# Optimization experiments

Hardware: AMD Instinct MI355X
Metric: run time of the kernel (lower is better)

Reference implementation:

```python
import jax, jax.numpy as jnp
import numpy as np

EPS_MAG = 1e-6    # magnitude threshold for valid trajectory
EPS_WSUM = 1e-8   # clamp on combined weight sum


def setup_inputs() -> dict:
    key = jax.random.key(0)
    embeddings = jax.random.normal(key, (4, 4096, 1024), dtype=jnp.float32)
    return {"embeddings": embeddings, "max_trajectory_distance": 8}


def reference(embeddings, max_trajectory_distance):
    # Vectorized form of compute_sparse_trajectories:
    # for each pos p >= 1, window of diffs d[start..p-1], start = max(0, p - max_dist),
    # normalized diffs weighted by linspace(0.1, 1.0, window) * tanh(2*|d|),
    # output[p] = weighted sum / clamp(weight sum, 1e-8); output[0] = 0.
    B, S, D = embeddings.shape
    maxd = min(int(max_trajectory_distance), S - 1)

    d = embeddings[:, 1:, :] - embeddings[:, :-1, :]            # [B, S-1, D]
    mag = jnp.linalg.norm(d, axis=-1)                           # [B, S-1]
    normed = jnp.where((mag > EPS_MAG)[..., None],
                       d / jnp.maximum(mag, EPS_MAG)[..., None],
                       0.0)                                     # [B, S-1, D]
    magw = jnp.tanh(mag * 2.0)                                  # [B, S-1]

    p = jnp.arange(S)                                           # positions
    wsize = jnp.minimum(maxd, p)                                # window size per pos
    j = jnp.arange(maxd)
    idx = p[:, None] - maxd + j[None, :]                        # [S, maxd] diff indices (end-aligned)
    valid = idx >= 0                                            # [S, maxd]
    # k = rank within window (0..wsize-1): weights linspace(0.1, 1.0, wsize)
    k = (j[None, :] - (maxd - wsize)[:, None]).astype(jnp.float32)
    denom = jnp.maximum(wsize - 1, 1).astype(jnp.float32)[:, None]
    lin = jnp.where(wsize[:, None] > 1, 0.1 + 0.9 * k / denom, 0.1)
    lin = jnp.where(valid, lin, 0.0)                            # [S, maxd]

    ci = jnp.clip(idx, 0, S - 2)                                # safe gather indices
    n_g = normed[:, ci, :]                                      # [B, S, maxd, D]
    m_g = magw[:, ci]                                           # [B, S, maxd]
    comb = lin[None, :, :] * m_g * valid[None, :, :]            # combined weights

    wsum = jnp.maximum(comb.sum(axis=-1), EPS_WSUM)             # [B, S]
    traj = jnp.einsum('bsjd,bsj->bsd', n_g, comb) / wsum[..., None]
    return traj
```

## Files before the change

### kernel.cpp

```cpp
#include <hip/hip_runtime.h>
#include <hip/hip_bf16.h>


constexpr int B_ = 4;
constexpr int S_ = 4096;
constexpr int D_ = 1024;
constexpr int MAXD  = 8;
constexpr int CHUNK = 32;
constexpr int ROWS  = CHUNK + MAXD;
constexpr int NDIFF = ROWS - 1;
constexpr int NCHUNK = S_ / CHUNK;
constexpr int NWG    = NCHUNK * B_;
constexpr int NXCD   = 8;

__global__ __launch_bounds__(256, 2)
void traj_splat_kernel(const float* __restrict__ emb, float* __restrict__ out) {
    const int bid = blockIdx.x;
    const int lin = (bid % NXCD) * (NWG / NXCD) + bid / NXCD;
    const int schunk = lin & (NCHUNK - 1);
    const int b      = lin >> 7;

    const int s0   = schunk * CHUNK;
    const int lane = threadIdx.x & 63;
    const int wave = threadIdx.x >> 6;
    const int d0   = threadIdx.x * 4;

    const float* __restrict__ embB = emb + (size_t)b * S_ * D_;

    __shared__ float part[NDIFF][4][4];
    __shared__ float smagw[NDIFF];
    __shared__ float sq[NDIFF];
    __shared__ float gco[CHUNK][12];

    float4 win[ROWS];
    #pragma unroll
    for (int r = 0; r < ROWS; ++r) {
        const int row = s0 - MAXD + r;
        if (row >= 0)
            win[r] = *(const float4*)(embB + (size_t)row * D_ + d0);
        else
            win[r] = make_float4(0.f, 0.f, 0.f, 0.f);
    }

    #pragma unroll
    for (int li = 0; li < NDIFF; ++li) {
        const float4 a = win[li], c = win[li + 1];
        const float dx = c.x - a.x, dy = c.y - a.y;
        const float dz = c.z - a.z, dw = c.w - a.w;
        float sum = dx * dx + dy * dy + dz * dz + dw * dw;
        sum += __shfl_xor(sum, 32, 64);
        sum += __shfl_xor(sum, 16, 64);
        sum += __shfl_xor(sum,  8, 64);
        sum += __shfl_xor(sum,  4, 64);
        if (lane < 4) part[li][wave][lane] = sum;
    }
    __syncthreads();

    if (threadIdx.x < NDIFF) {
        const int li = threadIdx.x;
        float s2 = 0.f;
        #pragma unroll
        for (int w = 0; w < 4; ++w)
            #pragma unroll
            for (int k = 0; k < 4; ++k)
                s2 += part[li][w][k];
        const float mag = sqrtf(s2);
        const float mw  = tanhf(2.f * mag);
        smagw[li] = mw;
        sq[li]    = (mag > 1e-6f) ? (mw / mag) : 0.f;
    }
    __syncthreads();

    if (threadIdx.x < CHUNK) {
        const int sl = threadIdx.x;
        const int s  = s0 + sl;
        const int ws = min(MAXD, s);
        const int lo = MAXD - ws;
        const float rden = 0.9f / (float)max(ws - 1, 1);

        float cpad[MAXD + 2];
        #pragma unroll
        for (int t = 0; t < MAXD + 2; ++t) cpad[t] = 0.f;

        float wsum = 0.f;
        #pragma unroll
        for (int j = 0; j < MAXD; ++j) {
            if (j >= lo) {
                const int li = sl + j;
                const float lin2 = (ws > 1) ? (0.1f + rden * (float)(j - lo)) : 0.1f;
                wsum += lin2 * smagw[li];
                cpad[j + 1] = lin2 * sq[li];
            }
        }
        const float inv = 1.f / fmaxf(wsum, 1e-8f);
        #pragma unroll
        for (int jr = 0; jr <= MAXD; ++jr)
            gco[sl][jr] = (cpad[jr] - cpad[jr + 1]) * inv;
    }
    __syncthreads();

    float* outB = out + ((size_t)b * S_ + s0) * D_ + d0;
    #pragma unroll
    for (int sl = 0; sl < CHUNK; ++sl) {
        const float4 g0 = *(const float4*)&gco[sl][0];
        const float4 g1 = *(const float4*)&gco[sl][4];
        const float  g8 = gco[sl][8];

        float4 acc;
        acc.x = g0.x * win[sl].x; acc.y = g0.x * win[sl].y;
        acc.z = g0.x * win[sl].z; acc.w = g0.x * win[sl].w;
        const float gs[8] = {g0.y, g0.z, g0.w, g1.x, g1.y, g1.z, g1.w, g8};
        #pragma unroll
        for (int jr = 1; jr <= MAXD; ++jr) {
            const float g = gs[jr - 1];
            acc.x += g * win[sl + jr].x;
            acc.y += g * win[sl + jr].y;
            acc.z += g * win[sl + jr].z;
            acc.w += g * win[sl + jr].w;
        }
        *(float4*)(outB + (size_t)sl * D_) = acc;
    }
}

extern "C" void kernel_launch(void* const* d_in, const int* in_sizes, int n_in,
                              void* d_out, int out_size, void* d_ws, size_t ws_size,
                              hipStream_t stream) {
    const float* emb = (const float*)d_in[0];
    float* out = (float*)d_out;

    dim3 grid(NWG);
    dim3 block(256);
    traj_splat_kernel<<<grid, block, 0, stream>>>(emb, out);
}
```

Before: 29.71 us.

## Split into magnitude pre-pass and splat kernel to drop halo recompute

Splits the fused kernel in two. A first pass computes each diff's magnitude weight and scale once and writes them to the workspace. A second kernel uses smaller 16-row chunks, reads those per-diff scalars from global memory, and does the weighted splat. This removes the redundant norm reductions over halo rows and allows higher occupancy, at the cost of an extra launch, a second full read of the embeddings, and a dependency on workspace size, with a fallback to the old fused kernel when the workspace is too small.

```diff
diff --git a/kernel.cpp b/kernel.cpp
--- a/kernel.cpp
+++ b/kernel.cpp
@@ -5,45 +5,36 @@
 constexpr int B_ = 4;
 constexpr int S_ = 4096;
 constexpr int D_ = 1024;
-constexpr int MAXD  = 8;
-constexpr int CHUNK = 32;
-constexpr int ROWS  = CHUNK + MAXD;
-constexpr int NDIFF = ROWS - 1;
-constexpr int NCHUNK = S_ / CHUNK;
-constexpr int NWG    = NCHUNK * B_;
-constexpr int NXCD   = 8;
+constexpr int MAXD = 8;
+constexpr int NDIFF_TOT = S_ - 1;
+
+constexpr int K1_CHUNK = 32;
 
 __global__ __launch_bounds__(256, 2)
-void traj_splat_kernel(const float* __restrict__ emb, float* __restrict__ out) {
-    const int bid = blockIdx.x;
-    const int lin = (bid % NXCD) * (NWG / NXCD) + bid / NXCD;
-    const int schunk = lin & (NCHUNK - 1);
-    const int b      = lin >> 7;
-
-    const int s0   = schunk * CHUNK;
+void mag_kernel(const float* __restrict__ emb,
+                float* __restrict__ magw_g, float* __restrict__ q_g) {
+    const int r0 = blockIdx.x * K1_CHUNK;
+    const int b  = blockIdx.y;
     const int lane = threadIdx.x & 63;
     const int wave = threadIdx.x >> 6;
     const int d0   = threadIdx.x * 4;
 
     const float* __restrict__ embB = emb + (size_t)b * S_ * D_;
 
-    __shared__ float part[NDIFF][4][4];
-    __shared__ float smagw[NDIFF];
-    __shared__ float sq[NDIFF];
-    __shared__ float gco[CHUNK][12];
-
-    float4 win[ROWS];
-    #pragma unroll
-    for (int r = 0; r < ROWS; ++r) {
-        const int row = s0 - MAXD + r;
-        if (row >= 0)
+    __shared__ float part[K1_CHUNK][4][4];
+
+    float4 win[K1_CHUNK + 1];
+    #pragma unroll
+    for (int r = 0; r <= K1_CHUNK; ++r) {
+        const int row = r0 + r;
+        if (row < S_)
             win[r] = *(const float4*)(embB + (size_t)row * D_ + d0);
         else
             win[r] = make_float4(0.f, 0.f, 0.f, 0.f);
     }
 
     #pragma unroll
-    for (int li = 0; li < NDIFF; ++li) {
+    for (int li = 0; li < K1_CHUNK; ++li) {
         const float4 a = win[li], c = win[li + 1];
         const float dx = c.x - a.x, dy = c.y - a.y;
         const float dz = c.z - a.z, dw = c.w - a.w;
@@ -56,7 +47,159 @@
     }
     __syncthreads();
 
-    if (threadIdx.x < NDIFF) {
+    if (threadIdx.x < K1_CHUNK) {
+        const int li = threadIdx.x;
+        const int d  = r0 + li;
+        if (d < NDIFF_TOT) {
+            float s2 = 0.f;
+            #pragma unroll
+            for (int w = 0; w < 4; ++w)
+                #pragma unroll
+                for (int k = 0; k < 4; ++k)
+                    s2 += part[li][w][k];
+            const float mag = sqrtf(s2);
+            const float mw  = tanhf(2.f * mag);
+            const size_t o  = (size_t)b * NDIFF_TOT + d;
+            magw_g[o] = mw;
+            q_g[o]    = (mag > 1e-6f) ? (mw / mag) : 0.f;
+        }
+    }
+}
+
+constexpr int CHUNK2  = 16;
+constexpr int ROWS2   = CHUNK2 + MAXD;
+constexpr int NCHUNK2 = S_ / CHUNK2;
+constexpr int NWG2    = NCHUNK2 * B_;
+constexpr int NXCD    = 8;
+
+__global__ __launch_bounds__(256, 3)
+void splat_kernel(const float* __restrict__ emb,
+                  const float* __restrict__ magw_g, const float* __restrict__ q_g,
+                  float* __restrict__ out) {
+    const int bid = blockIdx.x;
+    const int lin = (bid % NXCD) * (NWG2 / NXCD) + bid / NXCD;
+    const int schunk = lin & (NCHUNK2 - 1);
+    const int b      = lin >> 8;
+
+    const int s0 = schunk * CHUNK2;
+    const int d0 = threadIdx.x * 4;
+
+    const float* __restrict__ embB = emb + (size_t)b * S_ * D_;
+
+    __shared__ float gco[CHUNK2][12];
+
+    float4 win[ROWS2];
+    #pragma unroll
+    for (int r = 0; r < ROWS2; ++r) {
+        const int row = s0 - MAXD + r;
+        if (row >= 0)
+            win[r] = *(const float4*)(embB + (size_t)row * D_ + d0);
+        else
+            win[r] = make_float4(0.f, 0.f, 0.f, 0.f);
+    }
+
+    if (threadIdx.x < CHUNK2) {
+        const int sl = threadIdx.x;
+        const int s  = s0 + sl;
+        const int ws = min(MAXD, s);
+        const int lo = MAXD - ws;
+        const float rden = 0.9f / (float)max(ws - 1, 1);
+        const size_t bD  = (size_t)b * NDIFF_TOT;
+
+        float cpad[MAXD + 2];
+        #pragma unroll
+        for (int t = 0; t < MAXD + 2; ++t) cpad[t] = 0.f;
+
+        float wsum = 0.f;
+        #pragma unroll
+        for (int j = 0; j < MAXD; ++j) {
+            if (j >= lo) {
+                const int d = s - MAXD + j;
+                const float lin2 = (ws > 1) ? (0.1f + rden * (float)(j - lo)) : 0.1f;
+                wsum += lin2 * magw_g[bD + d];
+                cpad[j + 1] = lin2 * q_g[bD + d];
+            }
+        }
+        const float inv = 1.f / fmaxf(wsum, 1e-8f);
+        #pragma unroll
+        for (int jr = 0; jr <= MAXD; ++jr)
+            gco[sl][jr] = (cpad[jr] - cpad[jr + 1]) * inv;
+    }
+    __syncthreads();
+
+    float* outB = out + ((size_t)b * S_ + s0) * D_ + d0;
+    #pragma unroll
+    for (int sl = 0; sl < CHUNK2; ++sl) {
+        const float4 g0 = *(const float4*)&gco[sl][0];
+        const float4 g1 = *(const float4*)&gco[sl][4];
+        const float  g8 = gco[sl][8];
+
+        float4 acc;
+        acc.x = g0.x * win[sl].x; acc.y = g0.x * win[sl].y;
+        acc.z = g0.x * win[sl].z; acc.w = g0.x * win[sl].w;
+        const float gs[8] = {g0.y, g0.z, g0.w, g1.x, g1.y, g1.z, g1.w, g8};
+        #pragma unroll
+        for (int jr = 1; jr <= MAXD; ++jr) {
+            const float g = gs[jr - 1];
+            acc.x += g * win[sl + jr].x;
+            acc.y += g * win[sl + jr].y;
+            acc.z += g * win[sl + jr].z;
+            acc.w += g * win[sl + jr].w;
+        }
+        *(float4*)(outB + (size_t)sl * D_) = acc;
+    }
+}
+
+constexpr int FCHUNK = 32;
+constexpr int FROWS  = FCHUNK + MAXD;
+constexpr int FNDIFF = FROWS - 1;
+constexpr int FNCH   = S_ / FCHUNK;
+constexpr int FNWG   = FNCH * B_;
+
+__global__ __launch_bounds__(256, 2)
+void traj_splat_fallback(const float* __restrict__ emb, float* __restrict__ out) {
+    const int bid = blockIdx.x;
+    const int lin = (bid % NXCD) * (FNWG / NXCD) + bid / NXCD;
+    const int schunk = lin & (FNCH - 1);
+    const int b      = lin >> 7;
+
+    const int s0   = schunk * FCHUNK;
+    const int lane = threadIdx.x & 63;
+    const int wave = threadIdx.x >> 6;
+    const int d0   = threadIdx.x * 4;
+
+    const float* __restrict__ embB = emb + (size_t)b * S_ * D_;
+
+    __shared__ float part[FNDIFF][4][4];
+    __shared__ float smagw[FNDIFF];
+    __shared__ float sq[FNDIFF];
+    __shared__ float gco[FCHUNK][12];
+
+    float4 win[FROWS];
+    #pragma unroll
+    for (int r = 0; r < FROWS; ++r) {
+        const int row = s0 - MAXD + r;
+        if (row >= 0)
+            win[r] = *(const float4*)(embB + (size_t)row * D_ + d0);
+        else
+            win[r] = make_float4(0.f, 0.f, 0.f, 0.f);
+    }
+
+    #pragma unroll
+    for (int li = 0; li < FNDIFF; ++li) {
+        const float4 a = win[li], c = win[li + 1];
+        const float dx = c.x - a.x, dy = c.y - a.y;
+        const float dz = c.z - a.z, dw = c.w - a.w;
+        float sum = dx * dx + dy * dy + dz * dz + dw * dw;
+        sum += __shfl_xor(sum, 32, 64);
+        sum += __shfl_xor(sum, 16, 64);
+        sum += __shfl_xor(sum,  8, 64);
+        sum += __shfl_xor(sum,  4, 64);
+        if (lane < 4) part[li][wave][lane] = sum;
+    }
+    __syncthreads();
+
+    if (threadIdx.x < FNDIFF) {
         const int li = threadIdx.x;
         float s2 = 0.f;
         #pragma unroll
@@ -71,7 +214,7 @@
     }
     __syncthreads();
 
-    if (threadIdx.x < CHUNK) {
+    if (threadIdx.x < FCHUNK) {
         const int sl = threadIdx.x;
         const int s  = s0 + sl;
         const int ws = min(MAXD, s);
@@ -101,7 +244,7 @@
 
     float* outB = out + ((size_t)b * S_ + s0) * D_ + d0;
     #pragma unroll
-    for (int sl = 0; sl < CHUNK; ++sl) {
+    for (int sl = 0; sl < FCHUNK; ++sl) {
         const float4 g0 = *(const float4*)&gco[sl][0];
         const float4 g1 = *(const float4*)&gco[sl][4];
         const float  g8 = gco[sl][8];
@@ -128,7 +271,18 @@
     const float* emb = (const float*)d_in[0];
     float* out = (float*)d_out;
 
-    dim3 grid(NWG);
-    dim3 block(256);
-    traj_splat_kernel<<<grid, block, 0, stream>>>(emb, out);
-}
+    const size_t need = 2 * (size_t)B_ * NDIFF_TOT * sizeof(float);
+    if (ws_size >= need) {
+        float* magw_g = (float*)d_ws;
+        float* q_g    = magw_g + (size_t)B_ * NDIFF_TOT;
+
+        dim3 g1(S_ / K1_CHUNK, B_);
+        mag_kernel<<<g1, dim3(256), 0, stream>>>(emb, magw_g, q_g);
+
+        dim3 g2(NWG2);
+        splat_kernel<<<g2, dim3(256), 0, stream>>>(emb, magw_g, q_g, out);
+    } else {
+        dim3 g(FNWG);
+        traj_splat_fallback<<<g, dim3(256), 0, stream>>>(emb, out);
+    }
+}
```

Result: slower. 43.02 us (+44.8%).
